# Optimization experiments

Measured on AMD Instinct MI355X. Metric: run time of the kernel, lower is better.

## Reference

```python
import jax, jax.numpy as jnp
import numpy as np

NUM_HEADS = 32
NUM_KV_HEADS = 8
HEAD_DIM = 64


def rotate_half(x):
    x1, x2 = jnp.split(x, 2, axis=-1)
    return jnp.concatenate((-x2, x1), axis=-1)


def setup_inputs() -> dict:
    key = jax.random.key(0)
    ks = jax.random.split(key, 7)
    B, S, H = 2, 2048, 2048
    hidden_states = jax.random.normal(ks[0], (B, S, H), dtype=jnp.float32)
    # RoPE angles: build realistic cos/sin from inv_freq for positions 0..S-1
    inv_freq = 1.0 / (10000.0 ** (np.arange(0, HEAD_DIM, 2, dtype=np.float32) / HEAD_DIM))
    t = np.arange(S, dtype=np.float32)
    freqs = np.outer(t, inv_freq)  # [S, HEAD_DIM/2]
    emb = np.concatenate([freqs, freqs], axis=-1)  # [S, HEAD_DIM]
    cos = jnp.broadcast_to(jnp.cos(emb)[None], (B, S, HEAD_DIM)).astype(jnp.float32)
    sin = jnp.broadcast_to(jnp.sin(emb)[None], (B, S, HEAD_DIM)).astype(jnp.float32)
    scale = 1.0 / np.sqrt(H)
    Wq = jax.random.normal(ks[1], (NUM_HEADS * HEAD_DIM, H), dtype=jnp.float32) * scale
    Wk = jax.random.normal(ks[2], (NUM_KV_HEADS * HEAD_DIM, H), dtype=jnp.float32) * scale
    Wv = jax.random.normal(ks[3], (NUM_KV_HEADS * HEAD_DIM, H), dtype=jnp.float32) * scale
    Wo = jax.random.normal(ks[4], (H, H), dtype=jnp.float32) * scale
    return {"hidden_states": hidden_states, "cos": cos, "sin": sin,
            "Wq": Wq, "Wk": Wk, "Wv": Wv, "Wo": Wo}


def reference(hidden_states, cos, sin, Wq, Wk, Wv, Wo):
    B, S, H = hidden_states.shape
    hd = HEAD_DIM
    # QKV projections (torch Linear: y = x @ W.T)
    q = jnp.einsum('bsi,oi->bso', hidden_states, Wq).reshape(B, S, NUM_HEADS, hd).transpose(0, 2, 1, 3)
    k = jnp.einsum('bsi,oi->bso', hidden_states, Wk).reshape(B, S, NUM_KV_HEADS, hd).transpose(0, 2, 1, 3)
    v = jnp.einsum('bsi,oi->bso', hidden_states, Wv).reshape(B, S, NUM_KV_HEADS, hd).transpose(0, 2, 1, 3)
    # RoPE: cos/sin [B,S,hd] -> [B,1,S,hd] broadcast over heads
    c = cos[:, None, :, :]
    s = sin[:, None, :, :]
    q = q * c + rotate_half(q) * s
    k = k * c + rotate_half(k) * s
    # GQA: repeat kv heads to match query heads
    groups = NUM_HEADS // NUM_KV_HEADS
    k = jnp.repeat(k, groups, axis=1)
    v = jnp.repeat(v, groups, axis=1)
    scaling = hd ** -0.5
    scores = jnp.einsum('bhqd,bhkd->bhqk', q, k) * scaling
    causal = jnp.tril(jnp.ones((S, S), dtype=bool))
    scores = jnp.where(causal, scores, jnp.finfo(scores.dtype).min)
    attn = jax.nn.softmax(scores, axis=-1)
    y = jnp.einsum('bhqk,bhkd->bhqd', attn, v)
    y = y.transpose(0, 2, 1, 3).reshape(B, S, H)
    return jnp.einsum('bsi,oi->bso', y, Wo)
```

## Files before the change

kernel.cpp:

```cpp
#include <hip/hip_runtime.h>

typedef __bf16 bf16_t;
typedef bf16_t bf16x8 __attribute__((ext_vector_type(8)));
typedef bf16_t bf16x4 __attribute__((ext_vector_type(4)));
typedef float f32x4 __attribute__((ext_vector_type(4)));
typedef float f32x16 __attribute__((ext_vector_type(16)));

#define MFMA16(a, b, c) __builtin_amdgcn_mfma_f32_16x16x32_bf16(a, b, c, 0, 0, 0)
#define MFMA32(a, b, c) __builtin_amdgcn_mfma_f32_32x32x16_bf16(a, b, c, 0, 0, 0)

#define GLOAD16(gsrc, ldst)                                            \
  __builtin_amdgcn_global_load_lds(                                    \
      (const __attribute__((address_space(1))) void*)(gsrc),           \
      (__attribute__((address_space(3))) void*)(ldst), 16, 0, 0)

constexpr int B_ = 2, S_ = 2048, H_ = 2048, NH = 32, NKV = 8, HD = 64;
constexpr int NQKV = NH * HD + 2 * NKV * HD;
constexpr int M_ROWS = B_ * S_;
constexpr float QSCALE = 0.125f * 1.4426950408889634f;

__global__ __launch_bounds__(256) void cvt_all(const float* __restrict__ hs,
                                               const float* __restrict__ Wq,
                                               const float* __restrict__ Wk,
                                               const float* __restrict__ Wv,
                                               const float* __restrict__ Wo,
                                               bf16_t* __restrict__ hsb,
                                               bf16_t* __restrict__ wqkv,
                                               bf16_t* __restrict__ wo) {
  const long i = (long)blockIdx.x * 256 + threadIdx.x;
  const float* src;
  bf16_t* dst;
  if (i < 1048576) {
    src = hs + i * 8;            dst = hsb + i * 8;
  } else if (i < 1572864) {
    const long j = i - 1048576;  src = Wq + j * 8;  dst = wqkv + j * 8;
  } else if (i < 1703936) {
    const long j = i - 1572864;  src = Wk + j * 8;  dst = wqkv + 4194304 + j * 8;
  } else if (i < 1835008) {
    const long j = i - 1703936;  src = Wv + j * 8;  dst = wqkv + 5242880 + j * 8;
  } else {
    const long j = i - 1835008;  src = Wo + j * 8;  dst = wo + j * 8;
  }
  const float4* p = (const float4*)src;
  float4 a = p[0], b = p[1];
  bf16x8 o;
  o[0] = (bf16_t)a.x; o[1] = (bf16_t)a.y; o[2] = (bf16_t)a.z; o[3] = (bf16_t)a.w;
  o[4] = (bf16_t)b.x; o[5] = (bf16_t)b.y; o[6] = (bf16_t)b.z; o[7] = (bf16_t)b.w;
  *(bf16x8*)dst = o;
}

template <bool OUT_BF16>
__global__ __launch_bounds__(256) void gemm_bt(const bf16_t* __restrict__ A,
                                               const bf16_t* __restrict__ Bm,
                                               float* __restrict__ Cf,
                                               bf16_t* __restrict__ Cb,
                                               int M, int N, int K) {
  __shared__ __align__(16) bf16_t As[2][128 * 32];
  __shared__ __align__(16) bf16_t Bs[2][128 * 32];
  const int t = threadIdx.x;
  const int lane = t & 63, w = t >> 6;
  const int l15 = lane & 15, l4 = lane >> 4;
  const int wm = w >> 1, wn = w & 1;
  const long Ar0 = (long)blockIdx.y * 128;
  const long Br0 = (long)blockIdx.x * 128;
  const int nt = K >> 5;

  const int scol = ((lane & 3) ^ ((lane >> 3) & 3)) * 8;
  const int srow = lane >> 2;
  auto stage = [&](int kt, int buf) {
#pragma unroll
    for (int c = 0; c < 2; ++c) {
      const int i = w * 2 + c;
      const bf16_t* gA = A + (Ar0 + i * 16 + srow) * (long)K + kt * 32 + scol;
      const bf16_t* gB = Bm + (Br0 + i * 16 + srow) * (long)K + kt * 32 + scol;
      GLOAD16(gA, &As[buf][i * 512]);
      GLOAD16(gB, &Bs[buf][i * 512]);
    }
  };

  f32x4 acc[4][4] = {};
  stage(0, 0);
  __syncthreads();
  int cur = 0;
  const int rsw = l4 ^ ((l15 >> 1) & 3);
  for (int kt = 0; kt < nt; ++kt) {
    if (kt + 1 < nt) stage(kt + 1, cur ^ 1);
    bf16x8 af[4], bfr[4];
#pragma unroll
    for (int mf = 0; mf < 4; ++mf)
      af[mf] = *(const bf16x8*)&As[cur][(wm * 64 + mf * 16 + l15) * 32 + rsw * 8];
#pragma unroll
    for (int nf = 0; nf < 4; ++nf)
      bfr[nf] = *(const bf16x8*)&Bs[cur][(wn * 64 + nf * 16 + l15) * 32 + rsw * 8];
#pragma unroll
    for (int mf = 0; mf < 4; ++mf)
#pragma unroll
      for (int nf = 0; nf < 4; ++nf)
        acc[mf][nf] = MFMA16(af[mf], bfr[nf], acc[mf][nf]);
    __syncthreads();
    cur ^= 1;
  }
#pragma unroll
  for (int mf = 0; mf < 4; ++mf)
#pragma unroll
    for (int nf = 0; nf < 4; ++nf)
#pragma unroll
      for (int r = 0; r < 4; ++r) {
        long row = Ar0 + wm * 64 + mf * 16 + l4 * 4 + r;
        long col = Br0 + wn * 64 + nf * 16 + l15;
        float v = acc[mf][nf][r];
        if (OUT_BF16)
          Cb[row * N + col] = (bf16_t)v;
        else
          Cf[row * N + col] = v;
      }
}

__global__ __launch_bounds__(256) void rope_kernel(bf16_t* __restrict__ qkv,
                                                   const float* __restrict__ cosb,
                                                   const float* __restrict__ sinb) {
  const int head = blockIdx.y;
  const int i = blockIdx.x * 256 + threadIdx.x;
  const long bs = i >> 2;
  const int d0 = (i & 3) * 8;
  const long base = bs * NQKV + (head < 32 ? head * 64 : 2048 + (head - 32) * 64) + d0;
  const float scl = head < 32 ? QSCALE : 1.0f;
  bf16x8 x1 = *(bf16x8*)(qkv + base);
  bf16x8 x2 = *(bf16x8*)(qkv + base + 32);
  const float4* cp = (const float4*)(cosb + bs * 64 + d0);
  const float4* sp = (const float4*)(sinb + bs * 64 + d0);
  const float4 c0 = cp[0], c1 = cp[1];
  const float4 s0 = sp[0], s1 = sp[1];
  const float cc[8] = {c0.x, c0.y, c0.z, c0.w, c1.x, c1.y, c1.z, c1.w};
  const float ss[8] = {s0.x, s0.y, s0.z, s0.w, s1.x, s1.y, s1.z, s1.w};
  bf16x8 y1, y2;
#pragma unroll
  for (int e = 0; e < 8; ++e) {
    const float f1 = (float)x1[e], f2 = (float)x2[e];
    y1[e] = (bf16_t)((f1 * cc[e] - f2 * ss[e]) * scl);
    y2[e] = (bf16_t)((f2 * cc[e] + f1 * ss[e]) * scl);
  }
  *(bf16x8*)(qkv + base) = y1;
  *(bf16x8*)(qkv + base + 32) = y2;
}

__global__ __launch_bounds__(256) void v_transpose(const bf16_t* __restrict__ qkv,
                                                   bf16_t* __restrict__ vT) {
  __shared__ __align__(16) bf16_t lds[64 * 64];
  const int b = blockIdx.z, kvh = blockIdx.y, s0 = blockIdx.x * 64;
  const int t = threadIdx.x;
  auto key = [](int s) { return (((s & 7) ^ ((s >> 3) & 7)) << 3); };
  const int si = t >> 3, j8 = (t & 7) * 8;
  const bf16_t* src = qkv + ((long)(b * S_ + s0 + si)) * NQKV + 2560 + kvh * 64 + j8;
  *(bf16x8*)&lds[si * 64 + (j8 ^ key(si))] = *(const bf16x8*)src;
  *(bf16x8*)&lds[(si + 32) * 64 + (j8 ^ key(si + 32))] =
      *(const bf16x8*)(src + 32L * NQKV);
  __syncthreads();
  const int d = t >> 2, sg = (t & 3) * 16;
  bf16x8 o0, o1;
#pragma unroll
  for (int e = 0; e < 8; ++e) {
    o0[e] = lds[(sg + e) * 64 + (d ^ key(sg + e))];
    o1[e] = lds[(sg + 8 + e) * 64 + (d ^ key(sg + 8 + e))];
  }
  bf16_t* dst = vT + ((long)(b * NKV + kvh) * 64 + d) * S_ + s0 + sg;
  *(bf16x8*)dst = o0;
  *(bf16x8*)(dst + 8) = o1;
}

__device__ __forceinline__ unsigned pkbf16(float lo, float hi) {
  union { bf16_t h[2]; unsigned u; } x;
  x.h[0] = (bf16_t)lo;
  x.h[1] = (bf16_t)hi;
  return x.u;
}

__global__ __launch_bounds__(256, 4) void attn32_kernel(const bf16_t* __restrict__ qkv,
                                                        const bf16_t* __restrict__ vT,
                                                        bf16_t* __restrict__ y) {
  constexpr int LSTR = 72;
  const int bx = blockIdx.x;
  const int p = bx & 15;
  const int hp = (bx >> 4) & 1;
  const int kvh = (bx >> 5) & 7;
  const int b = bx >> 8;
  const int t = threadIdx.x, lane = t & 63, w = t >> 6;
  const int l31 = lane & 31, hd = lane >> 5;
  const int h = kvh * 4 + hp * 2 + (w >> 1);
  const long bS = (long)b * S_;

  __shared__ __align__(16) bf16_t Klds[2][64 * LSTR];
  __shared__ __align__(16) bf16_t Vlds[2][64 * LSTR];

  const bf16_t* kbase = qkv + bS * NQKV + NH * HD + kvh * 64;
  const bf16_t* vbase = vT + ((long)(b * NKV + kvh)) * 64 * S_;

  const int row0 = t >> 3, slot = t & 7;
  int woff[2];
#pragma unroll
  for (int c = 0; c < 2; ++c) woff[c] = (row0 + 32 * c) * LSTR + slot * 8;
  int roff[4][2];
#pragma unroll
  for (int ks = 0; ks < 4; ++ks)
#pragma unroll
    for (int kb = 0; kb < 2; ++kb)
      roff[ks][kb] = (kb * 32 + l31) * LSTR + (2 * ks + hd) * 8;

  const bf16_t* kp0[2];
  const bf16_t* vp0[2];
#pragma unroll
  for (int c = 0; c < 2; ++c) {
    kp0[c] = kbase + (long)(row0 + 32 * c) * NQKV + slot * 8;
    vp0[c] = vbase + (long)(row0 + 32 * c) * S_ + slot * 8;
  }

  bf16x8 kreg[2], vreg[2];

  for (int half = 0; half < 2; ++half) {
    const int qt = half ? p : 31 - p;
    const int q0w = qt * 64 + (w & 1) * 32;
    const int myq = q0w + l31;
    const int NT = qt + 1;

    const bf16_t* qp = qkv + (bS + myq) * NQKV + h * 64 + hd * 8;
    bf16x8 qf[4];
#pragma unroll
    for (int ks = 0; ks < 4; ++ks) qf[ks] = *(const bf16x8*)(qp + ks * 16);

    const bf16_t* kp[2];
    const bf16_t* vp[2];
#pragma unroll
    for (int c = 0; c < 2; ++c) { kp[c] = kp0[c]; vp[c] = vp0[c]; }

    auto ldG = [&]() {
#pragma unroll
      for (int c = 0; c < 2; ++c) {
        kreg[c] = *(const bf16x8*)kp[c];
        vreg[c] = *(const bf16x8*)vp[c];
        kp[c] += 64L * NQKV;
        vp[c] += 64;
      }
    };
    auto wrLDS = [&](int buf) {
#pragma unroll
      for (int c = 0; c < 2; ++c) {
        *(bf16x8*)&Klds[buf][woff[c]] = kreg[c];
        *(bf16x8*)&Vlds[buf][woff[c]] = vreg[c];
      }
    };

    f32x16 yac[2] = {};
    float m = -1e30f, l = 0.f;

    ldG();
    wrLDS(0);
    __syncthreads();

    for (int kt = 0; kt < NT; ++kt) {
      const int buf = kt & 1;
      const int kv0 = kt * 64;
      if (kt + 1 < NT) ldG();

      const bf16_t* Kb = &Klds[buf][0];
      const bf16_t* Vb = &Vlds[buf][0];

      f32x16 sac[2] = {};
      __builtin_amdgcn_s_setprio(1);
#pragma unroll
      for (int ks = 0; ks < 4; ++ks)
#pragma unroll
        for (int kb = 0; kb < 2; ++kb)
          sac[kb] = MFMA32(*(const bf16x8*)&Kb[roff[ks][kb]], qf[ks], sac[kb]);
      __builtin_amdgcn_s_setprio(0);
      if (kv0 + 63 > q0w) {
#pragma unroll
        for (int kb = 0; kb < 2; ++kb)
#pragma unroll
          for (int r = 0; r < 16; ++r) {
            const int kv = kv0 + kb * 32 + (r & 3) + 8 * (r >> 2) + 4 * hd;
            if (kv > myq) sac[kb][r] = -3.0e38f;
          }
      }
      float pm4[8], sm4[8];
#pragma unroll
      for (int g = 0; g < 8; ++g) {
        const int kb = g >> 2, r = (g & 3) * 4;
        pm4[g] = fmaxf(fmaxf(sac[kb][r], sac[kb][r + 1]),
                       fmaxf(sac[kb][r + 2], sac[kb][r + 3]));
      }
      float pm = fmaxf(fmaxf(fmaxf(pm4[0], pm4[1]), fmaxf(pm4[2], pm4[3])),
                       fmaxf(fmaxf(pm4[4], pm4[5]), fmaxf(pm4[6], pm4[7])));
      pm = fmaxf(pm, __shfl_xor(pm, 32, 64));
      if (!__all(pm <= m + 8.f)) {
        const float mnew = fmaxf(m, pm);
        const float sc = __builtin_amdgcn_exp2f(m - mnew);
        l *= sc;
        yac[0] *= sc;
        yac[1] *= sc;
        m = mnew;
      }
#pragma unroll
      for (int kb = 0; kb < 2; ++kb)
#pragma unroll
        for (int r = 0; r < 16; ++r)
          sac[kb][r] = __builtin_amdgcn_exp2f(sac[kb][r] - m);
#pragma unroll
      for (int g = 0; g < 8; ++g) {
        const int kb = g >> 2, r = (g & 3) * 4;
        sm4[g] = (sac[kb][r] + sac[kb][r + 1]) + (sac[kb][r + 2] + sac[kb][r + 3]);
      }
      l += ((sm4[0] + sm4[1]) + (sm4[2] + sm4[3])) +
           ((sm4[4] + sm4[5]) + (sm4[6] + sm4[7]));
#pragma unroll
      for (int ks = 0; ks < 4; ++ks) {
        const int kb = ks >> 1;
        const int Bv = 8 * (ks & 1);
        unsigned a0 = pkbf16(sac[kb][Bv + 0], sac[kb][Bv + 1]);
        unsigned b0 = pkbf16(sac[kb][Bv + 4], sac[kb][Bv + 5]);
        unsigned a1 = pkbf16(sac[kb][Bv + 2], sac[kb][Bv + 3]);
        unsigned b1 = pkbf16(sac[kb][Bv + 6], sac[kb][Bv + 7]);
        asm("v_permlane32_swap_b32 %0, %1" : "+v"(a0), "+v"(b0));
        asm("v_permlane32_swap_b32 %0, %1" : "+v"(a1), "+v"(b1));
        union { unsigned u[4]; bf16x8 v; } pu;
        pu.u[0] = a0; pu.u[1] = a1; pu.u[2] = b0; pu.u[3] = b1;
        __builtin_amdgcn_s_setprio(1);
#pragma unroll
        for (int db = 0; db < 2; ++db)
          yac[db] = MFMA32(*(const bf16x8*)&Vb[roff[ks][db]], pu.v, yac[db]);
        __builtin_amdgcn_s_setprio(0);
      }

      if (kt + 1 < NT) wrLDS(buf ^ 1);
      __syncthreads();
    }

    l += __shfl_xor(l, 32, 64);
    const float inv = __builtin_amdgcn_rcpf(l);
    bf16_t* yp = y + (bS + myq) * (long)H_ + h * 64;
#pragma unroll
    for (int db = 0; db < 2; ++db)
#pragma unroll
      for (int g = 0; g < 4; ++g) {
        bf16x4 o;
        o[0] = (bf16_t)(yac[db][4 * g + 0] * inv);
        o[1] = (bf16_t)(yac[db][4 * g + 1] * inv);
        o[2] = (bf16_t)(yac[db][4 * g + 2] * inv);
        o[3] = (bf16_t)(yac[db][4 * g + 3] * inv);
        *(bf16x4*)(yp + db * 32 + 8 * g + 4 * hd) = o;
      }
  }
}

extern "C" void kernel_launch(void* const* d_in, const int* in_sizes, int n_in,
                              void* d_out, int out_size, void* d_ws, size_t ws_size,
                              hipStream_t stream) {
  const float* hs = (const float*)d_in[0];
  const float* cosb = (const float*)d_in[1];
  const float* sinb = (const float*)d_in[2];
  const float* Wq = (const float*)d_in[3];
  const float* Wk = (const float*)d_in[4];
  const float* Wv = (const float*)d_in[5];
  const float* Wo = (const float*)d_in[6];
  float* out = (float*)d_out;

  char* ws = (char*)d_ws;
  bf16_t* hsb  = (bf16_t*)(ws);
  bf16_t* wqkv = (bf16_t*)(ws + 16777216);
  bf16_t* wo   = (bf16_t*)(ws + 29360128);
  bf16_t* qkv  = (bf16_t*)(ws + 37748736);
  bf16_t* vT   = (bf16_t*)(ws + 62914560);
  bf16_t* yb   = (bf16_t*)(ws + 67108864);

  cvt_all<<<9216, 256, 0, stream>>>(hs, Wq, Wk, Wv, Wo, hsb, wqkv, wo);

  gemm_bt<true><<<dim3(24, 32), 256, 0, stream>>>(hsb, wqkv, nullptr, qkv,
                                                  M_ROWS, NQKV, H_);
  rope_kernel<<<dim3(64, 40), 256, 0, stream>>>(qkv, cosb, sinb);
  v_transpose<<<dim3(32, 8, 2), 256, 0, stream>>>(qkv, vT);
  attn32_kernel<<<512, 256, 0, stream>>>(qkv, vT, yb);
  gemm_bt<false><<<dim3(16, 32), 256, 0, stream>>>(yb, wo, out, nullptr,
                                                   M_ROWS, H_, H_);
}
```

Baseline: 206.8 us.

## Split attention work per head across warps handling paired causal tiles

```diff
diff --git a/kernel.cpp b/kernel.cpp
--- a/kernel.cpp
+++ b/kernel.cpp
@@ -180,13 +180,12 @@
                                                         bf16_t* __restrict__ y) {
   constexpr int LSTR = 72;
   const int bx = blockIdx.x;
-  const int p = bx & 15;
-  const int hp = (bx >> 4) & 1;
-  const int kvh = (bx >> 5) & 7;
-  const int b = bx >> 8;
+  const int h = bx & 31;
+  const int p = (bx >> 5) & 15;
+  const int b = bx >> 9;
+  const int kvh = h >> 2;
   const int t = threadIdx.x, lane = t & 63, w = t >> 6;
   const int l31 = lane & 31, hd = lane >> 5;
-  const int h = kvh * 4 + hp * 2 + (w >> 1);
   const long bS = (long)b * S_;
 
   __shared__ __align__(16) bf16_t Klds[2][64 * LSTR];
@@ -206,61 +205,49 @@
     for (int kb = 0; kb < 2; ++kb)
       roff[ks][kb] = (kb * 32 + l31) * LSTR + (2 * ks + hd) * 8;
 
-  const bf16_t* kp0[2];
-  const bf16_t* vp0[2];
-#pragma unroll
-  for (int c = 0; c < 2; ++c) {
-    kp0[c] = kbase + (long)(row0 + 32 * c) * NQKV + slot * 8;
-    vp0[c] = vbase + (long)(row0 + 32 * c) * S_ + slot * 8;
-  }
+  const bf16_t* kp = kbase + (long)(row0)*NQKV + slot * 8;
+  const bf16_t* vp = vbase + (long)(row0)*S_ + slot * 8;
+  const long kstep2 = 32L * NQKV, vstep2 = 32L * S_;
 
   bf16x8 kreg[2], vreg[2];
-
-  for (int half = 0; half < 2; ++half) {
-    const int qt = half ? p : 31 - p;
-    const int q0w = qt * 64 + (w & 1) * 32;
-    const int myq = q0w + l31;
-    const int NT = qt + 1;
-
-    const bf16_t* qp = qkv + (bS + myq) * NQKV + h * 64 + hd * 8;
-    bf16x8 qf[4];
-#pragma unroll
-    for (int ks = 0; ks < 4; ++ks) qf[ks] = *(const bf16x8*)(qp + ks * 16);
-
-    const bf16_t* kp[2];
-    const bf16_t* vp[2];
-#pragma unroll
-    for (int c = 0; c < 2; ++c) { kp[c] = kp0[c]; vp[c] = vp0[c]; }
-
-    auto ldG = [&]() {
-#pragma unroll
-      for (int c = 0; c < 2; ++c) {
-        kreg[c] = *(const bf16x8*)kp[c];
-        vreg[c] = *(const bf16x8*)vp[c];
-        kp[c] += 64L * NQKV;
-        vp[c] += 64;
-      }
-    };
-    auto wrLDS = [&](int buf) {
-#pragma unroll
-      for (int c = 0; c < 2; ++c) {
-        *(bf16x8*)&Klds[buf][woff[c]] = kreg[c];
-        *(bf16x8*)&Vlds[buf][woff[c]] = vreg[c];
-      }
-    };
-
-    f32x16 yac[2] = {};
-    float m = -1e30f, l = 0.f;
-
-    ldG();
-    wrLDS(0);
-    __syncthreads();
-
-    for (int kt = 0; kt < NT; ++kt) {
-      const int buf = kt & 1;
-      const int kv0 = kt * 64;
-      if (kt + 1 < NT) ldG();
-
+  auto ldG = [&]() {
+    kreg[0] = *(const bf16x8*)kp;
+    kreg[1] = *(const bf16x8*)(kp + kstep2);
+    vreg[0] = *(const bf16x8*)vp;
+    vreg[1] = *(const bf16x8*)(vp + vstep2);
+    kp += 64L * NQKV;
+    vp += 64;
+  };
+  auto wrLDS = [&](int buf) {
+    *(bf16x8*)&Klds[buf][woff[0]] = kreg[0];
+    *(bf16x8*)&Klds[buf][woff[1]] = kreg[1];
+    *(bf16x8*)&Vlds[buf][woff[0]] = vreg[0];
+    *(bf16x8*)&Vlds[buf][woff[1]] = vreg[1];
+  };
+
+  const int qt = (w < 2) ? 31 - p : p;
+  const int q0w = qt * 64 + (w & 1) * 32;
+  const int myq = q0w + l31;
+  const int NT = 32 - p;
+
+  const bf16_t* qp = qkv + (bS + myq) * NQKV + h * 64 + hd * 8;
+  bf16x8 qf[4];
+#pragma unroll
+  for (int ks = 0; ks < 4; ++ks) qf[ks] = *(const bf16x8*)(qp + ks * 16);
+
+  f32x16 yac[2] = {};
+  float m = -1e30f, l = 0.f;
+
+  ldG();
+  wrLDS(0);
+  __syncthreads();
+
+  for (int kt = 0; kt < NT; ++kt) {
+    const int buf = kt & 1;
+    const int kv0 = kt * 64;
+    if (kt + 1 < NT) ldG();
+
+    if (kv0 <= q0w + 31) {
       const bf16_t* Kb = &Klds[buf][0];
       const bf16_t* Vb = &Vlds[buf][0];
 
@@ -329,26 +316,26 @@
           yac[db] = MFMA32(*(const bf16x8*)&Vb[roff[ks][db]], pu.v, yac[db]);
         __builtin_amdgcn_s_setprio(0);
       }
-
-      if (kt + 1 < NT) wrLDS(buf ^ 1);
-      __syncthreads();
     }
 
-    l += __shfl_xor(l, 32, 64);
-    const float inv = __builtin_amdgcn_rcpf(l);
-    bf16_t* yp = y + (bS + myq) * (long)H_ + h * 64;
-#pragma unroll
-    for (int db = 0; db < 2; ++db)
-#pragma unroll
-      for (int g = 0; g < 4; ++g) {
-        bf16x4 o;
-        o[0] = (bf16_t)(yac[db][4 * g + 0] * inv);
-        o[1] = (bf16_t)(yac[db][4 * g + 1] * inv);
-        o[2] = (bf16_t)(yac[db][4 * g + 2] * inv);
-        o[3] = (bf16_t)(yac[db][4 * g + 3] * inv);
-        *(bf16x4*)(yp + db * 32 + 8 * g + 4 * hd) = o;
-      }
-  }
+    if (kt + 1 < NT) wrLDS(buf ^ 1);
+    __syncthreads();
+  }
+
+  l += __shfl_xor(l, 32, 64);
+  const float inv = __builtin_amdgcn_rcpf(l);
+  bf16_t* yp = y + (bS + myq) * (long)H_ + h * 64;
+#pragma unroll
+  for (int db = 0; db < 2; ++db)
+#pragma unroll
+    for (int g = 0; g < 4; ++g) {
+      bf16x4 o;
+      o[0] = (bf16_t)(yac[db][4 * g + 0] * inv);
+      o[1] = (bf16_t)(yac[db][4 * g + 1] * inv);
+      o[2] = (bf16_t)(yac[db][4 * g + 2] * inv);
+      o[3] = (bf16_t)(yac[db][4 * g + 3] * inv);
+      *(bf16x4*)(yp + db * 32 + 8 * g + 4 * hd) = o;
+    }
 }
 
 extern "C" void kernel_launch(void* const* d_in, const int* in_sizes, int n_in,
@@ -377,7 +364,7 @@
                                                   M_ROWS, NQKV, H_);
   rope_kernel<<<dim3(64, 40), 256, 0, stream>>>(qkv, cosb, sinb);
   v_transpose<<<dim3(32, 8, 2), 256, 0, stream>>>(qkv, vT);
-  attn32_kernel<<<512, 256, 0, stream>>>(qkv, vT, yb);
+  attn32_kernel<<<1024, 256, 0, stream>>>(qkv, vT, yb);
   gemm_bt<false><<<dim3(16, 32), 256, 0, stream>>>(yb, wo, out, nullptr,
                                                    M_ROWS, H_, H_);
 }
```

New measurement: 211.0 us. +2.0%, slower.
